# Kernel tuning notes

Measured on AMD Instinct MI355X. Metric: run time of the kernel, lower is better.

## Reference

```python
import jax, jax.numpy as jnp
import numpy as np
import math

N_NODES = 100000
N_EDGES = 1600000
INPUT_SIZE = 256
N_HEADS = 8
HEAD_SIZE = INPUT_SIZE // N_HEADS  # 32
DK = math.sqrt(HEAD_SIZE)


def setup_inputs() -> dict:
    key = jax.random.key(0)
    k1, k2, k3, k4, k5 = jax.random.split(key, 5)
    X = jax.random.normal(k1, (N_NODES, INPUT_SIZE), dtype=jnp.float32)
    edge_index = jax.random.randint(k2, (2, N_EDGES), 0, N_NODES, dtype=jnp.int64)
    # kaiming_normal (fan_in = input_size) std = sqrt(2/fan_in)
    std = math.sqrt(2.0 / INPUT_SIZE)
    Wq = jax.random.normal(k3, (INPUT_SIZE, HEAD_SIZE), dtype=jnp.float32) * std
    Wk = jax.random.normal(k4, (INPUT_SIZE, HEAD_SIZE), dtype=jnp.float32) * std
    Wv = jax.random.normal(k5, (INPUT_SIZE, HEAD_SIZE), dtype=jnp.float32) * std
    return {"X": X, "edge_index": edge_index, "Wq": Wq, "Wk": Wk, "Wv": Wv}


def reference(X, edge_index, Wq, Wk, Wv):
    N = X.shape[0]
    Q = X @ Wq  # [N, h]
    K = X @ Wk  # [N, h]
    V = X @ Wv  # [N, h]
    src = edge_index[0]  # row index (softmax over dim=1 -> per-src segments)
    dst = edge_index[1]
    # per-edge QK dot, scaled
    scores = jnp.sum(Q[src] * K[dst], axis=-1) / DK  # [E]
    # segment-wise (sparse) softmax over each row
    row_max = jax.ops.segment_max(scores, src, num_segments=N)  # [N]
    ex = jnp.exp(scores - row_max[src])  # [E]
    denom = jax.ops.segment_sum(ex, src, num_segments=N)  # [N]
    alpha = ex / denom[src]  # [E]
    # sparse-mm aggregate of V: out[i] = sum_j alpha_ij * V[j]
    out = jax.ops.segment_sum(alpha[:, None] * V[dst], src, num_segments=N)  # [N, h]
    return out
```

## Files before the change

kernel.cpp:

```cpp
#include <hip/hip_runtime.h>

#define N_INPUT 256
#define HS 32

#define BKT_SHIFT 7
#define BKT_NODES 128
#define NBUCK_MAX 800
#define CAP 2560
#define EPB 4096
#define S1_THREADS 512

typedef __attribute__((ext_vector_type(8))) short bf16x8;
typedef __attribute__((ext_vector_type(4))) float f32x4;
typedef __attribute__((ext_vector_type(8))) unsigned short u16x8;

__device__ __forceinline__ unsigned short f2bf(float f) {
    unsigned u = __float_as_uint(f);
    unsigned r = u + 0x7FFFu + ((u >> 16) & 1u);
    return (unsigned short)(r >> 16);
}
__device__ __forceinline__ float bf2f(unsigned short u) {
    return __uint_as_float((unsigned)u << 16);
}


__global__ void zero_gtail_kernel(int* __restrict__ gtail, int nb,
                                  int* __restrict__ rowstart, int N, int E) {
    int t = threadIdx.x;
    for (int i = t; i < nb; i += 256) gtail[i] = 0;
    if (t == 0) rowstart[N] = E;
}

__global__ __launch_bounds__(S1_THREADS) void s1_partition_kernel(
        const int* __restrict__ src, const int* __restrict__ dst,
        int* __restrict__ gtail, uint2* __restrict__ staging, int E, int nb) {
    __shared__ int h[NBUCK_MAX];
    __shared__ int bs[NBUCK_MAX];
    __shared__ int rk[NBUCK_MAX];
    int t = threadIdx.x;
    int e0 = blockIdx.x * EPB;
    int lim = min(EPB, E - e0);
    for (int i = t; i < nb; i += S1_THREADS) { h[i] = 0; rk[i] = 0; }
    __syncthreads();
    for (int i = t; i < lim; i += S1_THREADS) {
        int b = src[e0 + i] >> BKT_SHIFT;
        atomicAdd(&h[b], 1);
    }
    __syncthreads();
    for (int b = t; b < nb; b += S1_THREADS) {
        int c = h[b];
        bs[b] = c ? atomicAdd(&gtail[b], c) : 0;
    }
    __syncthreads();
    for (int i = t; i < lim; i += S1_THREADS) {
        int s = src[e0 + i];
        int d = dst[e0 + i];
        int b = s >> BKT_SHIFT;
        int r = atomicAdd(&rk[b], 1);
        int pos = bs[b] + r;
        if (pos < CAP)
            staging[(size_t)b * CAP + pos] = make_uint2((unsigned)s, (unsigned)d);
    }
}

__global__ __launch_bounds__(256) void s2_build_kernel(
        const uint2* __restrict__ staging, const int* __restrict__ gtail,
        int* __restrict__ rowstart, int* __restrict__ sorted_dst, int N, int nb) {
    __shared__ uint2 se[CAP];
    __shared__ int nh[BKT_NODES];
    __shared__ int nx[BKT_NODES];
    __shared__ int rk[BKT_NODES];
    __shared__ int red[256];
    int b = blockIdx.x;
    int t = threadIdx.x;
    int partial = 0;
    for (int i = t; i < b; i += 256) partial += min(gtail[i], CAP);
    red[t] = partial;
    if (t < BKT_NODES) { nh[t] = 0; rk[t] = 0; }
    __syncthreads();
    for (int off = 128; off > 0; off >>= 1) {
        if (t < off) red[t] += red[t + off];
        __syncthreads();
    }
    int gbase = red[0];
    int cnt = min(gtail[b], CAP);
    int node0 = b << BKT_SHIFT;
    for (int i = t; i < cnt; i += 256) {
        uint2 e = staging[(size_t)b * CAP + i];
        se[i] = e;
        atomicAdd(&nh[e.x & (BKT_NODES - 1)], 1);
    }
    __syncthreads();
    if (t < BKT_NODES) nx[t] = nh[t];
    __syncthreads();
    for (int off = 1; off < BKT_NODES; off <<= 1) {
        int u = (t >= off && t < BKT_NODES) ? nx[t - off] : 0;
        __syncthreads();
        if (t < BKT_NODES) nx[t] += u;
        __syncthreads();
    }
    if (t < BKT_NODES) {
        int node = node0 + t;
        if (node < N) rowstart[node] = gbase + nx[t] - nh[t];
    }
    __syncthreads();
    for (int i = t; i < cnt; i += 256) {
        uint2 e = se[i];
        int sl = (int)(e.x & (BKT_NODES - 1));
        int r = atomicAdd(&rk[sl], 1);
        sorted_dst[gbase + nx[sl] - nh[sl] + r] = (int)e.y;
    }
}

__global__ __launch_bounds__(256) void qkv_mfma_kernel(
        const float* __restrict__ X, const float* __restrict__ Wq,
        const float* __restrict__ Wk, const float* __restrict__ Wv,
        float* __restrict__ Q, unsigned short* __restrict__ KVb, int N) {
    __shared__ unsigned short sB[6 * 8 * 64 * 8];

    int tid = threadIdx.x;
    for (int i = 0; i < 12; ++i) {
        int c = tid + i * 256;
        int s = c >> 9;
        int t = (c >> 6) & 7;
        int L = c & 63;
        const float* wm = (s < 2) ? Wq : (s < 4) ? Wk : Wv;
        const float* wsrc = wm + (size_t)(t * 32 + (L >> 4) * 8) * HS + (s & 1) * 16 + (L & 15);
        unsigned e0 = f2bf(wsrc[0 * HS]) | ((unsigned)f2bf(wsrc[1 * HS]) << 16);
        unsigned e1 = f2bf(wsrc[2 * HS]) | ((unsigned)f2bf(wsrc[3 * HS]) << 16);
        unsigned e2 = f2bf(wsrc[4 * HS]) | ((unsigned)f2bf(wsrc[5 * HS]) << 16);
        unsigned e3 = f2bf(wsrc[6 * HS]) | ((unsigned)f2bf(wsrc[7 * HS]) << 16);
        ((uint4*)sB)[c] = make_uint4(e0, e1, e2, e3);
    }
    __syncthreads();

    int wave = tid >> 6;
    int L = tid & 63;
    int quad = L >> 4;
    int lane16 = L & 15;
    int mt = blockIdx.x * 4 + wave;
    if (mt * 16 >= N) return;

    const float* xrow = X + (size_t)(mt * 16 + lane16) * N_INPUT + quad * 8;
    bf16x8 afrag[8];
#pragma unroll
    for (int t = 0; t < 8; ++t) {
        float4 a0 = *(const float4*)(xrow + t * 32);
        float4 a1 = *(const float4*)(xrow + t * 32 + 4);
        bf16x8 f;
        f[0] = (short)f2bf(a0.x); f[1] = (short)f2bf(a0.y);
        f[2] = (short)f2bf(a0.z); f[3] = (short)f2bf(a0.w);
        f[4] = (short)f2bf(a1.x); f[5] = (short)f2bf(a1.y);
        f[6] = (short)f2bf(a1.z); f[7] = (short)f2bf(a1.w);
        afrag[t] = f;
    }

#pragma unroll
    for (int s = 0; s < 6; ++s) {
        f32x4 acc = {0.f, 0.f, 0.f, 0.f};
#pragma unroll
        for (int t = 0; t < 8; ++t) {
            bf16x8 bfrag = *((const bf16x8*)sB + (s * 8 + t) * 64 + L);
            acc = __builtin_amdgcn_mfma_f32_16x16x32_bf16(afrag[t], bfrag, acc, 0, 0, 0);
        }
        int col = (s & 1) * 16 + lane16;
#pragma unroll
        for (int r = 0; r < 4; ++r) {
            int row = mt * 16 + quad * 4 + r;
            if (s < 2) {
                Q[(size_t)row * HS + col] = acc[r];
            } else {
                size_t pos = (size_t)row * 64 + (size_t)(col >> 2) * 8 +
                             ((s < 4) ? 0 : 4) + (col & 3);
                KVb[pos] = f2bf(acc[r]);
            }
        }
    }
}

__global__ __launch_bounds__(256) void fused_agg_kernel(
        const int* __restrict__ rowstart, const int* __restrict__ sorted_dst,
        const float* __restrict__ Q, const unsigned short* __restrict__ KVb,
        float* __restrict__ out, int N) {
    int lane = threadIdx.x & 31;
    int n = blockIdx.x * 8 + (threadIdx.x >> 5);
    if (n >= N) return;
    int slot = lane >> 3;
    int sub = lane & 7;
    int beg = rowstart[n], end = rowstart[n + 1];
    float4 qf = *(const float4*)(Q + (size_t)n * HS + sub * 4);
    float4 acc = make_float4(0.f, 0.f, 0.f, 0.f);
    float den = 0.f;

    for (int j = beg; j < end; j += 4) {
        int e = j + slot;
        bool valid = e < end;
        int d = 0;
        if (valid) d = sorted_dst[e];
        u16x8 kv = *(const u16x8*)(KVb + (size_t)d * 64 + sub * 8);
        float p = qf.x * bf2f(kv[0]) + qf.y * bf2f(kv[1]) +
                  qf.z * bf2f(kv[2]) + qf.w * bf2f(kv[3]);
        p += __shfl_xor(p, 1, 32);
        p += __shfl_xor(p, 2, 32);
        p += __shfl_xor(p, 4, 32);
        float ex = valid ? __expf(p * 0.17677669529663687f) : 0.f;
        den += ex;
        acc.x += ex * bf2f(kv[4]);
        acc.y += ex * bf2f(kv[5]);
        acc.z += ex * bf2f(kv[6]);
        acc.w += ex * bf2f(kv[7]);
    }
#pragma unroll
    for (int off = 8; off <= 16; off <<= 1) {
        acc.x += __shfl_xor(acc.x, off, 32);
        acc.y += __shfl_xor(acc.y, off, 32);
        acc.z += __shfl_xor(acc.z, off, 32);
        acc.w += __shfl_xor(acc.w, off, 32);
        den += __shfl_xor(den, off, 32);
    }
    if (lane < 8) {
        float4 o = make_float4(0.f, 0.f, 0.f, 0.f);
        if (end > beg) {
            float rd = 1.f / den;
            o = make_float4(acc.x * rd, acc.y * rd, acc.z * rd, acc.w * rd);
        }
        *(float4*)(out + (size_t)n * HS + lane * 4) = o;
    }
}

extern "C" void kernel_launch(void* const* d_in, const int* in_sizes, int n_in,
                              void* d_out, int out_size, void* d_ws, size_t ws_size,
                              hipStream_t stream) {
    const float* X  = (const float*)d_in[0];
    const int*   ei = (const int*)d_in[1];
    const float* Wq = (const float*)d_in[2];
    const float* Wk = (const float*)d_in[3];
    const float* Wv = (const float*)d_in[4];

    int N = in_sizes[0] / N_INPUT;
    int E = in_sizes[1] / 2;
    const int* src = ei;
    const int* dst = ei + E;

    float* ws = (float*)d_ws;
    float* Q = ws;
    unsigned short* KVb = (unsigned short*)(Q + (size_t)N * HS);
    int* rowstart = (int*)(KVb + (size_t)N * 64);
    int* sorted_dst = rowstart + N + 4;
    int* gtail = sorted_dst + E;
    uint2* staging = (uint2*)d_ws;
    float* out = (float*)d_out;

    int nbuck = (N + BKT_NODES - 1) >> BKT_SHIFT;

    zero_gtail_kernel<<<1, 256, 0, stream>>>(gtail, nbuck, rowstart, N, E);
    s1_partition_kernel<<<(E + EPB - 1) / EPB, S1_THREADS, 0, stream>>>(
        src, dst, gtail, staging, E, nbuck);
    s2_build_kernel<<<nbuck, 256, 0, stream>>>(
        staging, gtail, rowstart, sorted_dst, N, nbuck);

    int mtiles = (N + 15) / 16;
    qkv_mfma_kernel<<<(mtiles + 3) / 4, 256, 0, stream>>>(X, Wq, Wk, Wv, Q, KVb, N);

    fused_agg_kernel<<<(N + 7) / 8, 256, 0, stream>>>(rowstart, sorted_dst, Q, KVb, out, N);
}
```

Baseline: 269.7 us.

## Merge partition with QKV projection and fuse bucket sort into aggregation

Result: faster. 248.8 us (-7.7%).

```diff
diff --git a/kernel.cpp b/kernel.cpp
--- a/kernel.cpp
+++ b/kernel.cpp
@@ -7,8 +7,7 @@
 #define BKT_NODES 128
 #define NBUCK_MAX 800
 #define CAP 2560
-#define EPB 4096
-#define S1_THREADS 512
+#define EPB 2048
 
 typedef __attribute__((ext_vector_type(8))) short bf16x8;
 typedef __attribute__((ext_vector_type(4))) float f32x4;
@@ -23,102 +22,62 @@
     return __uint_as_float((unsigned)u << 16);
 }
 
-
-__global__ void zero_gtail_kernel(int* __restrict__ gtail, int nb,
-                                  int* __restrict__ rowstart, int N, int E) {
+__global__ void zero_gtail_kernel(int* __restrict__ gtail, int nb) {
     int t = threadIdx.x;
     for (int i = t; i < nb; i += 256) gtail[i] = 0;
-    if (t == 0) rowstart[N] = E;
-}
-
-__global__ __launch_bounds__(S1_THREADS) void s1_partition_kernel(
-        const int* __restrict__ src, const int* __restrict__ dst,
-        int* __restrict__ gtail, uint2* __restrict__ staging, int E, int nb) {
-    __shared__ int h[NBUCK_MAX];
-    __shared__ int bs[NBUCK_MAX];
-    __shared__ int rk[NBUCK_MAX];
-    int t = threadIdx.x;
-    int e0 = blockIdx.x * EPB;
-    int lim = min(EPB, E - e0);
-    for (int i = t; i < nb; i += S1_THREADS) { h[i] = 0; rk[i] = 0; }
-    __syncthreads();
-    for (int i = t; i < lim; i += S1_THREADS) {
-        int b = src[e0 + i] >> BKT_SHIFT;
-        atomicAdd(&h[b], 1);
-    }
-    __syncthreads();
-    for (int b = t; b < nb; b += S1_THREADS) {
-        int c = h[b];
-        bs[b] = c ? atomicAdd(&gtail[b], c) : 0;
-    }
-    __syncthreads();
-    for (int i = t; i < lim; i += S1_THREADS) {
-        int s = src[e0 + i];
-        int d = dst[e0 + i];
-        int b = s >> BKT_SHIFT;
-        int r = atomicAdd(&rk[b], 1);
-        int pos = bs[b] + r;
-        if (pos < CAP)
-            staging[(size_t)b * CAP + pos] = make_uint2((unsigned)s, (unsigned)d);
-    }
-}
-
-__global__ __launch_bounds__(256) void s2_build_kernel(
-        const uint2* __restrict__ staging, const int* __restrict__ gtail,
-        int* __restrict__ rowstart, int* __restrict__ sorted_dst, int N, int nb) {
-    __shared__ uint2 se[CAP];
-    __shared__ int nh[BKT_NODES];
-    __shared__ int nx[BKT_NODES];
-    __shared__ int rk[BKT_NODES];
-    __shared__ int red[256];
-    int b = blockIdx.x;
-    int t = threadIdx.x;
-    int partial = 0;
-    for (int i = t; i < b; i += 256) partial += min(gtail[i], CAP);
-    red[t] = partial;
-    if (t < BKT_NODES) { nh[t] = 0; rk[t] = 0; }
-    __syncthreads();
-    for (int off = 128; off > 0; off >>= 1) {
-        if (t < off) red[t] += red[t + off];
-        __syncthreads();
-    }
-    int gbase = red[0];
-    int cnt = min(gtail[b], CAP);
-    int node0 = b << BKT_SHIFT;
-    for (int i = t; i < cnt; i += 256) {
-        uint2 e = staging[(size_t)b * CAP + i];
-        se[i] = e;
-        atomicAdd(&nh[e.x & (BKT_NODES - 1)], 1);
-    }
-    __syncthreads();
-    if (t < BKT_NODES) nx[t] = nh[t];
-    __syncthreads();
-    for (int off = 1; off < BKT_NODES; off <<= 1) {
-        int u = (t >= off && t < BKT_NODES) ? nx[t - off] : 0;
-        __syncthreads();
-        if (t < BKT_NODES) nx[t] += u;
-        __syncthreads();
-    }
-    if (t < BKT_NODES) {
-        int node = node0 + t;
-        if (node < N) rowstart[node] = gbase + nx[t] - nh[t];
-    }
-    __syncthreads();
-    for (int i = t; i < cnt; i += 256) {
-        uint2 e = se[i];
-        int sl = (int)(e.x & (BKT_NODES - 1));
-        int r = atomicAdd(&rk[sl], 1);
-        sorted_dst[gbase + nx[sl] - nh[sl] + r] = (int)e.y;
-    }
-}
-
-__global__ __launch_bounds__(256) void qkv_mfma_kernel(
+}
+
+union MegaSmem {
+    unsigned short sB[6 * 8 * 64 * 8];
+    struct { int h[NBUCK_MAX]; int bs[NBUCK_MAX]; } p;
+};
+
+__global__ __launch_bounds__(256) void mega_kernel(
         const float* __restrict__ X, const float* __restrict__ Wq,
         const float* __restrict__ Wk, const float* __restrict__ Wv,
-        float* __restrict__ Q, unsigned short* __restrict__ KVb, int N) {
-    __shared__ unsigned short sB[6 * 8 * 64 * 8];
-
+        const int* __restrict__ src, const int* __restrict__ dst,
+        float* __restrict__ Q, unsigned short* __restrict__ KVb,
+        int* __restrict__ gtail, uint2* __restrict__ staging,
+        int N, int E, int nb, int s1blocks) {
+    __shared__ MegaSmem u;
     int tid = threadIdx.x;
+
+    if ((int)blockIdx.x < s1blocks) {
+        int e0 = blockIdx.x * EPB;
+        for (int i = tid; i < nb; i += 256) u.p.h[i] = 0;
+        __syncthreads();
+        int ss[8], dd[8], rr[8];
+#pragma unroll
+        for (int k = 0; k < 8; ++k) {
+            int i = e0 + tid + k * 256;
+            ss[k] = -1;
+            if (i < E) {
+                int s = src[i];
+                dd[k] = dst[i];
+                ss[k] = s;
+                rr[k] = atomicAdd(&u.p.h[s >> BKT_SHIFT], 1);
+            }
+        }
+        __syncthreads();
+        for (int b = tid; b < nb; b += 256) {
+            int c = u.p.h[b];
+            u.p.bs[b] = c ? atomicAdd(&gtail[b], c) : 0;
+        }
+        __syncthreads();
+#pragma unroll
+        for (int k = 0; k < 8; ++k) {
+            if (ss[k] >= 0) {
+                int b = ss[k] >> BKT_SHIFT;
+                int pos = u.p.bs[b] + rr[k];
+                if (pos < CAP)
+                    staging[(size_t)b * CAP + pos] =
+                        make_uint2((unsigned)ss[k], (unsigned)dd[k]);
+            }
+        }
+        return;
+    }
+
+    int bq = blockIdx.x - s1blocks;
     for (int i = 0; i < 12; ++i) {
         int c = tid + i * 256;
         int s = c >> 9;
@@ -130,7 +89,7 @@
         unsigned e1 = f2bf(wsrc[2 * HS]) | ((unsigned)f2bf(wsrc[3 * HS]) << 16);
         unsigned e2 = f2bf(wsrc[4 * HS]) | ((unsigned)f2bf(wsrc[5 * HS]) << 16);
         unsigned e3 = f2bf(wsrc[6 * HS]) | ((unsigned)f2bf(wsrc[7 * HS]) << 16);
-        ((uint4*)sB)[c] = make_uint4(e0, e1, e2, e3);
+        ((uint4*)u.sB)[c] = make_uint4(e0, e1, e2, e3);
     }
     __syncthreads();
 
@@ -138,7 +97,7 @@
     int L = tid & 63;
     int quad = L >> 4;
     int lane16 = L & 15;
-    int mt = blockIdx.x * 4 + wave;
+    int mt = bq * 4 + wave;
     if (mt * 16 >= N) return;
 
     const float* xrow = X + (size_t)(mt * 16 + lane16) * N_INPUT + quad * 8;
@@ -160,7 +119,7 @@
         f32x4 acc = {0.f, 0.f, 0.f, 0.f};
 #pragma unroll
         for (int t = 0; t < 8; ++t) {
-            bf16x8 bfrag = *((const bf16x8*)sB + (s * 8 + t) * 64 + L);
+            bf16x8 bfrag = *((const bf16x8*)u.sB + (s * 8 + t) * 64 + L);
             acc = __builtin_amdgcn_mfma_f32_16x16x32_bf16(afrag[t], bfrag, acc, 0, 0, 0);
         }
         int col = (s & 1) * 16 + lane16;
@@ -178,53 +137,96 @@
     }
 }
 
-__global__ __launch_bounds__(256) void fused_agg_kernel(
-        const int* __restrict__ rowstart, const int* __restrict__ sorted_dst,
+__global__ __launch_bounds__(512) void s2_agg_kernel(
+        const uint2* __restrict__ staging, const int* __restrict__ gtail,
         const float* __restrict__ Q, const unsigned short* __restrict__ KVb,
         float* __restrict__ out, int N) {
-    int lane = threadIdx.x & 31;
-    int n = blockIdx.x * 8 + (threadIdx.x >> 5);
-    if (n >= N) return;
+    __shared__ int ldst[CAP];
+    __shared__ int nh[BKT_NODES];
+    __shared__ int nx[BKT_NODES];
+    __shared__ int rk[BKT_NODES];
+    int b = blockIdx.x;
+    int t = threadIdx.x;
+    int cnt = min(gtail[b], CAP);
+    if (t < BKT_NODES) { nh[t] = 0; rk[t] = 0; }
+    __syncthreads();
+    uint2 stash[5];
+#pragma unroll
+    for (int k = 0; k < 5; ++k) {
+        int i = t + k * 512;
+        if (i < cnt) {
+            uint2 e = staging[(size_t)b * CAP + i];
+            stash[k] = e;
+            atomicAdd(&nh[e.x & (BKT_NODES - 1)], 1);
+        }
+    }
+    __syncthreads();
+    if (t < BKT_NODES) nx[t] = nh[t];
+    __syncthreads();
+    for (int off = 1; off < BKT_NODES; off <<= 1) {
+        int u = (t >= off && t < BKT_NODES) ? nx[t - off] : 0;
+        __syncthreads();
+        if (t < BKT_NODES) nx[t] += u;
+        __syncthreads();
+    }
+#pragma unroll
+    for (int k = 0; k < 5; ++k) {
+        int i = t + k * 512;
+        if (i < cnt) {
+            uint2 e = stash[k];
+            int sl = (int)(e.x & (BKT_NODES - 1));
+            int r = atomicAdd(&rk[sl], 1);
+            ldst[nx[sl] - nh[sl] + r] = (int)e.y;
+        }
+    }
+    __syncthreads();
+
+    int lane = t & 31;
+    int grp = t >> 5;
     int slot = lane >> 3;
     int sub = lane & 7;
-    int beg = rowstart[n], end = rowstart[n + 1];
-    float4 qf = *(const float4*)(Q + (size_t)n * HS + sub * 4);
-    float4 acc = make_float4(0.f, 0.f, 0.f, 0.f);
-    float den = 0.f;
-
-    for (int j = beg; j < end; j += 4) {
-        int e = j + slot;
-        bool valid = e < end;
-        int d = 0;
-        if (valid) d = sorted_dst[e];
-        u16x8 kv = *(const u16x8*)(KVb + (size_t)d * 64 + sub * 8);
-        float p = qf.x * bf2f(kv[0]) + qf.y * bf2f(kv[1]) +
-                  qf.z * bf2f(kv[2]) + qf.w * bf2f(kv[3]);
-        p += __shfl_xor(p, 1, 32);
-        p += __shfl_xor(p, 2, 32);
-        p += __shfl_xor(p, 4, 32);
-        float ex = valid ? __expf(p * 0.17677669529663687f) : 0.f;
-        den += ex;
-        acc.x += ex * bf2f(kv[4]);
-        acc.y += ex * bf2f(kv[5]);
-        acc.z += ex * bf2f(kv[6]);
-        acc.w += ex * bf2f(kv[7]);
-    }
-#pragma unroll
-    for (int off = 8; off <= 16; off <<= 1) {
-        acc.x += __shfl_xor(acc.x, off, 32);
-        acc.y += __shfl_xor(acc.y, off, 32);
-        acc.z += __shfl_xor(acc.z, off, 32);
-        acc.w += __shfl_xor(acc.w, off, 32);
-        den += __shfl_xor(den, off, 32);
-    }
-    if (lane < 8) {
-        float4 o = make_float4(0.f, 0.f, 0.f, 0.f);
-        if (end > beg) {
-            float rd = 1.f / den;
-            o = make_float4(acc.x * rd, acc.y * rd, acc.z * rd, acc.w * rd);
-        }
-        *(float4*)(out + (size_t)n * HS + lane * 4) = o;
+    int node0 = b << BKT_SHIFT;
+    for (int ni = grp; ni < BKT_NODES; ni += 16) {
+        int n = node0 + ni;
+        if (n >= N) continue;
+        int end = nx[ni];
+        int beg = end - nh[ni];
+        float4 qf = *(const float4*)(Q + (size_t)n * HS + sub * 4);
+        float4 acc = make_float4(0.f, 0.f, 0.f, 0.f);
+        float den = 0.f;
+        for (int j = beg; j < end; j += 4) {
+            int e = j + slot;
+            bool valid = e < end;
+            int d = valid ? ldst[e] : 0;
+            u16x8 kv = *(const u16x8*)(KVb + (size_t)d * 64 + sub * 8);
+            float p = qf.x * bf2f(kv[0]) + qf.y * bf2f(kv[1]) +
+                      qf.z * bf2f(kv[2]) + qf.w * bf2f(kv[3]);
+            p += __shfl_xor(p, 1, 32);
+            p += __shfl_xor(p, 2, 32);
+            p += __shfl_xor(p, 4, 32);
+            float ex = valid ? __expf(p * 0.17677669529663687f) : 0.f;
+            den += ex;
+            acc.x += ex * bf2f(kv[4]);
+            acc.y += ex * bf2f(kv[5]);
+            acc.z += ex * bf2f(kv[6]);
+            acc.w += ex * bf2f(kv[7]);
+        }
+#pragma unroll
+        for (int off = 8; off <= 16; off <<= 1) {
+            acc.x += __shfl_xor(acc.x, off, 32);
+            acc.y += __shfl_xor(acc.y, off, 32);
+            acc.z += __shfl_xor(acc.z, off, 32);
+            acc.w += __shfl_xor(acc.w, off, 32);
+            den += __shfl_xor(den, off, 32);
+        }
+        if (lane < 8) {
+            float4 o = make_float4(0.f, 0.f, 0.f, 0.f);
+            if (end > beg) {
+                float rd = 1.f / den;
+                o = make_float4(acc.x * rd, acc.y * rd, acc.z * rd, acc.w * rd);
+            }
+            *(float4*)(out + (size_t)n * HS + lane * 4) = o;
+        }
     }
 }
 
@@ -245,22 +247,17 @@
     float* ws = (float*)d_ws;
     float* Q = ws;
     unsigned short* KVb = (unsigned short*)(Q + (size_t)N * HS);
-    int* rowstart = (int*)(KVb + (size_t)N * 64);
-    int* sorted_dst = rowstart + N + 4;
-    int* gtail = sorted_dst + E;
-    uint2* staging = (uint2*)d_ws;
+    int* gtail = (int*)(KVb + (size_t)N * 64);
+    uint2* staging = (uint2*)(gtail + NBUCK_MAX);
     float* out = (float*)d_out;
 
     int nbuck = (N + BKT_NODES - 1) >> BKT_SHIFT;
-
-    zero_gtail_kernel<<<1, 256, 0, stream>>>(gtail, nbuck, rowstart, N, E);
-    s1_partition_kernel<<<(E + EPB - 1) / EPB, S1_THREADS, 0, stream>>>(
-        src, dst, gtail, staging, E, nbuck);
-    s2_build_kernel<<<nbuck, 256, 0, stream>>>(
-        staging, gtail, rowstart, sorted_dst, N, nbuck);
-
+    int s1blocks = (E + EPB - 1) / EPB;
     int mtiles = (N + 15) / 16;
-    qkv_mfma_kernel<<<(mtiles + 3) / 4, 256, 0, stream>>>(X, Wq, Wk, Wv, Q, KVb, N);
-
-    fused_agg_kernel<<<(N + 7) / 8, 256, 0, stream>>>(rowstart, sorted_dst, Q, KVb, out, N);
-}
+    int qblocks = (mtiles + 3) / 4;
+
+    zero_gtail_kernel<<<1, 256, 0, stream>>>(gtail, nbuck);
+    mega_kernel<<<s1blocks + qblocks, 256, 0, stream>>>(
+        X, Wq, Wk, Wv, src, dst, Q, KVb, gtail, staging, N, E, nbuck, s1blocks);
+    s2_agg_kernel<<<nbuck, 512, 0, stream>>>(staging, gtail, Q, KVb, out, N);
+}
```
